# Kernel tuning notes

Hardware: AMD Instinct MI355X
Metric: run time of the kernel (lower is better)

## Reference

```python
import jax, jax.numpy as jnp
import numpy as np

H = 512          # HIDDEN_DIM
W = 480          # WINDOWWIDTH
NL = 8           # NUMLABELS (output_dim)
STEPS = W // 15  # 32 decoder steps
ATT = W // 16    # 30 attention positions
B = 4            # window batch
L = 12           # per-frame sequence length
D_IN = 32        # input_dim
N = B * W        # 1920 frame sequences


def _lstm(x, Wih, Whh, bih, bhh):
    # x: [T, Bn, Din] -> per-step hidden/cell states [T, Bn, Hd] (torch LSTM gate order i,f,g,o)
    xp = x @ Wih.T + (bih + bhh)
    h0 = jnp.zeros((x.shape[1], Whh.shape[1]), x.dtype)
    def step(carry, xt):
        h, c = carry
        g = xt + h @ Whh.T
        i, f, gg, o = jnp.split(g, 4, axis=-1)
        c = jax.nn.sigmoid(f) * c + jax.nn.sigmoid(i) * jnp.tanh(gg)
        h = jax.nn.sigmoid(o) * jnp.tanh(c)
        return (h, c), (h, c)
    _, (hs, cs) = jax.lax.scan(step, (h0, h0), xp)
    return hs, cs


def _bilstm(x, Wf, Uf, bf, cf, Wb, Ub, bb, cb):
    # x: [Bt, T, D] batch_first; returns ([Bt, T, 2H], h_fwd_final, h_bwd_final)
    xt = jnp.swapaxes(x, 0, 1)
    hf, _ = _lstm(xt, Wf, Uf, bf, cf)
    hb, _ = _lstm(xt[::-1], Wb, Ub, bb, cb)
    out = jnp.concatenate([hf, hb[::-1]], axis=-1)
    return jnp.swapaxes(out, 0, 1), hf[-1], hb[-1]


def _forward(xs, xlengths, enc_Wih, enc_Whh, enc_bih, enc_bhh,
             penc_Wih_f, penc_Whh_f, penc_bih_f, penc_bhh_f,
             penc_Wih_b, penc_Whh_b, penc_bih_b, penc_bhh_b,
             attn_W, attn_b, comb_W, comb_b,
             gru_Wih, gru_Whh, gru_bih, gru_bhh, out_W, out_b):
    # frame-level encoder: packed sequences -> (h, c) at each sequence's true length
    hs, cs = _lstm(xs, enc_Wih, enc_Whh, enc_bih, enc_bhh)   # [L, N, H] each
    idx = xlengths - 1
    ar = jnp.arange(N)
    ctx = jnp.concatenate([hs[idx, ar], cs[idx, ar]], axis=-1)  # [N, 2H]
    ctx = ctx.reshape(B, W // 2, 4 * H)
    # pyramidal BiLSTM stack (dropout is identity at eval)
    out = ctx
    hf = hb = None
    for i in range(4):
        out, hf, hb = _bilstm(ctx, penc_Wih_f[i], penc_Whh_f[i], penc_bih_f[i], penc_bhh_f[i],
                              penc_Wih_b[i], penc_Whh_b[i], penc_bih_b[i], penc_bhh_b[i])
        if i < 3:
            ctx = out.reshape(B, W // (2 ** (i + 2)), 4 * H)
    enc_out = out                                   # [B, ATT, 2H]
    hidden0 = jnp.concatenate([hf, hb], axis=-1)    # [B, 2H]

    def dstep(carry, _):
        inp, h = carry                              # [B, NL], [B, 2H]
        aw = jax.nn.softmax(jnp.concatenate([inp, h], axis=-1) @ attn_W.T + attn_b, axis=-1)
        ctxv = jnp.einsum('bt,btd->bd', aw, enc_out)
        x = jax.nn.relu(jnp.concatenate([inp, ctxv], axis=-1) @ comb_W.T + comb_b)
        # torch GRU cell (gate order r, z, n)
        gi = x @ gru_Wih.T + gru_bih
        gh = h @ gru_Whh.T + gru_bhh
        ir, iz, inn = jnp.split(gi, 3, axis=-1)
        hr, hz, hn = jnp.split(gh, 3, axis=-1)
        r = jax.nn.sigmoid(ir + hr)
        z = jax.nn.sigmoid(iz + hz)
        n = jnp.tanh(inn + r * hn)
        hnew = (1.0 - z) * n + z * h
        logp = jax.nn.log_softmax(hnew @ out_W.T + out_b, axis=-1)
        return (logp, hnew), logp                   # free-running: next input = log-probs

    inp0 = jnp.zeros((B, NL), xs.dtype)
    _, outs = jax.lax.scan(dstep, (inp0, hidden0), None, length=STEPS)  # [STEPS, B, NL]
    return jnp.swapaxes(outs, 0, 1).reshape(B * STEPS, NL)


def setup_inputs() -> dict:
    key = jax.random.key(0)
    ks = jax.random.split(key, 24)
    s = 0.03
    def nrm(k, shape):
        return jax.random.normal(k, shape, dtype=jnp.float32) * s
    return {
        'xs': jax.random.normal(ks[0], (L, N, D_IN), dtype=jnp.float32),
        'xlengths': jax.random.randint(ks[1], (N,), 1, L + 1, dtype=jnp.int32),
        'enc_Wih': nrm(ks[2], (4 * H, D_IN)),
        'enc_Whh': nrm(ks[3], (4 * H, H)),
        'enc_bih': nrm(ks[4], (4 * H,)),
        'enc_bhh': nrm(ks[5], (4 * H,)),
        'penc_Wih_f': nrm(ks[6], (4, 4 * H, 4 * H)),
        'penc_Whh_f': nrm(ks[7], (4, 4 * H, H)),
        'penc_bih_f': nrm(ks[8], (4, 4 * H)),
        'penc_bhh_f': nrm(ks[9], (4, 4 * H)),
        'penc_Wih_b': nrm(ks[10], (4, 4 * H, 4 * H)),
        'penc_Whh_b': nrm(ks[11], (4, 4 * H, H)),
        'penc_bih_b': nrm(ks[12], (4, 4 * H)),
        'penc_bhh_b': nrm(ks[13], (4, 4 * H)),
        'attn_W': nrm(ks[14], (ATT, 2 * H + NL)),
        'attn_b': nrm(ks[15], (ATT,)),
        'comb_W': nrm(ks[16], (H, 2 * H + NL)),
        'comb_b': nrm(ks[17], (H,)),
        'gru_Wih': nrm(ks[18], (3 * 2 * H, H)),
        'gru_Whh': nrm(ks[19], (3 * 2 * H, 2 * H)),
        'gru_bih': nrm(ks[20], (3 * 2 * H,)),
        'gru_bhh': nrm(ks[21], (3 * 2 * H,)),
        'out_W': nrm(ks[22], (NL, 2 * H)),
        'out_b': nrm(ks[23], (NL,)),
    }


def reference(xs, xlengths, enc_Wih, enc_Whh, enc_bih, enc_bhh,
              penc_Wih_f, penc_Whh_f, penc_bih_f, penc_bhh_f,
              penc_Wih_b, penc_Whh_b, penc_bih_b, penc_bhh_b,
              attn_W, attn_b, comb_W, comb_b,
              gru_Wih, gru_Whh, gru_bih, gru_bhh, out_W, out_b):
    return _forward(xs, xlengths, enc_Wih, enc_Whh, enc_bih, enc_bhh,
                    penc_Wih_f, penc_Whh_f, penc_bih_f, penc_bhh_f,
                    penc_Wih_b, penc_Whh_b, penc_bih_b, penc_bhh_b,
                    attn_W, attn_b, comb_W, comb_b,
                    gru_Wih, gru_Whh, gru_bih, gru_bhh, out_W, out_b)
```

## Files before the change

kernel.cpp:

```cpp
#include <hip/hip_runtime.h>
#include <stdint.h>

typedef __attribute__((ext_vector_type(8))) __bf16 bf16x8;
typedef __attribute__((ext_vector_type(4))) float f32x4;
typedef __attribute__((ext_vector_type(4))) unsigned u32x4;

#define DEVI static __device__ __forceinline__
#define SENT 0xFFFFFFFFu

DEVI bf16x8 bzero8(){ bf16x8 r;
#pragma unroll
  for (int i=0;i<8;++i) r[i]=(__bf16)0.0f; return r; }

DEVI bf16x8 ld8(const __bf16* p){ return *(const bf16x8*)p; }
DEVI void st8(__bf16* p, bf16x8 v){ *(bf16x8*)p = v; }

DEVI f32x4 MFMA(bf16x8 a, bf16x8 b, f32x4 c){
  return __builtin_amdgcn_mfma_f32_16x16x32_bf16(a, b, c, 0, 0, 0);
}

DEVI float sigf(float x){ return 1.0f/(1.0f+__expf(-x)); }

DEVI void ast(unsigned* p, unsigned v){ __hip_atomic_store(p, v, __ATOMIC_RELAXED, __HIP_MEMORY_SCOPE_AGENT); }

DEVI unsigned packbf(float a, float b){
  union { __bf16 h[2]; unsigned u; } x; x.h[0]=(__bf16)a; x.h[1]=(__bf16)b; return x.u;
}
DEVI float bflo(unsigned u){ return __builtin_bit_cast(float, u<<16); }
DEVI float bfhi(unsigned u){ return __builtin_bit_cast(float, u & 0xffff0000u); }

DEVI unsigned bad4(u32x4 v){ return (v[0]==SENT)|(v[1]==SENT)|(v[2]==SENT)|(v[3]==SENT); }

DEVI u32x4 ald4(const void* p){
  u32x4 v;
  asm volatile("global_load_dwordx4 %0, %1, off sc0 sc1\n\ts_waitcnt vmcnt(0)"
               : "=&v"(v) : "v"(p) : "memory");
  return v;
}
DEVI u32x4 poll4(const void* p){
  u32x4 v = ald4(p);
  while (bad4(v)){ __builtin_amdgcn_s_sleep(1); v = ald4(p); }
  return v;
}
DEVI void ald4x2(const void* p, u32x4& a, u32x4& b){
  asm volatile("global_load_dwordx4 %0, %2, off sc0 sc1\n\t"
               "global_load_dwordx4 %1, %2, off offset:16 sc0 sc1\n\t"
               "s_waitcnt vmcnt(0)"
               : "=&v"(a), "=&v"(b) : "v"(p) : "memory");
}
DEVI void poll4x2(const void* p, u32x4& a, u32x4& b){
  ald4x2(p, a, b);
  while (bad4(a) | bad4(b)){ __builtin_amdgcn_s_sleep(1); ald4x2(p, a, b); }
}

DEVI void packGroup(const float* W, int Nsrc, int Kreal, int NT, __bf16* dst, long g){
  int kt = (int)(g / (NT*64));
  int rem = (int)(g % (NT*64));
  int nt = rem >> 6, ln = rem & 63;
  int row = nt*16 + (ln & 15);
  int col = kt*32 + ((ln >> 4) << 3);
  bf16x8 v = bzero8();
  if (row < Nsrc){
#pragma unroll
    for (int j=0;j<8;++j){ int c = col + j; if (c < Kreal) v[j] = (__bf16)W[(long)row*Kreal + c]; }
  }
  st8(dst + g*8, v);
}

DEVI void packGroupCat(const float* Wih, const float* Whh, __bf16* dst, long g){
  int kt = (int)(g / (128*64));
  int rem = (int)(g % (128*64));
  int nt = rem >> 6, ln = rem & 63;
  int prow = nt*16 + (ln & 15);
  int src = (prow & 3)*512 + (prow >> 2);
  int col = kt*32 + ((ln >> 4) << 3);
  bf16x8 v;
  if (col < 32){
#pragma unroll
    for (int j=0;j<8;++j) v[j] = (__bf16)Wih[(long)src*32 + col + j];
  } else {
#pragma unroll
    for (int j=0;j<8;++j) v[j] = (__bf16)Whh[(long)src*512 + (col-32) + j];
  }
  st8(dst + g*8, v);
}

__global__ void initK(unsigned* hb){
  int g = blockIdx.x*256 + threadIdx.x;
  if (g < 6144) hb[2048 + g] = SENT;
}

__global__ void packSmallK(const float* __restrict__ xs, const float* __restrict__ eWih,
    const float* __restrict__ eWhh, const float* __restrict__ ebih, const float* __restrict__ ebhh,
    const float* __restrict__ attnW,
    __bf16* __restrict__ xsb, __bf16* __restrict__ wcatp, float* __restrict__ biasc,
    __bf16* __restrict__ attnp)
{
  long g = (long)blockIdx.x*blockDim.x + threadIdx.x;
  const long nWcat = 17L*128*64;
  const long nXs   = 92160;
  const long nBias = 2048;
  const long nAttn = 33L*2*64;
  if (g < nWcat){ packGroupCat(eWih, eWhh, wcatp, g); return; }
  g -= nWcat;
  if (g < nXs){
    const float* s = xs + g*8; bf16x8 v;
#pragma unroll
    for (int j=0;j<8;++j) v[j] = (__bf16)s[j];
    st8(xsb + g*8, v); return;
  }
  g -= nXs;
  if (g < nBias){ int src = ((int)g & 3)*512 + ((int)g >> 2); biasc[g] = ebih[src] + ebhh[src]; return; }
  g -= nBias;
  if (g < nAttn){ packGroup(attnW, 30, 1032, 2, attnp, g); return; }
}

__global__ void packPencK(const float* __restrict__ Wf, const float* __restrict__ Wb,
    const float* __restrict__ WhF, const float* __restrict__ WhB,
    const float* __restrict__ bihf, const float* __restrict__ bhhf,
    const float* __restrict__ bihb, const float* __restrict__ bhhb,
    __bf16* __restrict__ pf, __bf16* __restrict__ pb, float* __restrict__ bsum,
    __bf16* __restrict__ pwhh, unsigned* __restrict__ hpy)
{
  long g = (long)blockIdx.x*blockDim.x + threadIdx.x;
  const long nW = 64L*128*64;
  if (g < nW){ packGroup(Wf, 2048, 2048, 128, pf, g); return; }
  g -= nW;
  if (g < nW){ packGroup(Wb, 2048, 2048, 128, pb, g); return; }
  g -= nW;
  if (g < 2048){ bsum[g] = bihf[g] + bhhf[g]; return; }
  g -= 2048;
  if (g < 2048){ bsum[2048+g] = bihb[g] + bhhb[g]; return; }
  g -= 2048;
  if (g < 8192){
    hpy[g] = ((g >> 10) & 3) ? SENT : 0u;
    return;
  }
  g -= 8192;
  if (g < 262144){
    int lane = (int)(g & 63);
    int f    = (int)((g >> 6) & 31);
    int w    = (int)((g >> 11) & 3);
    int slot = (int)((g >> 13) & 15);
    int dir  = (int)((g >> 17) & 1);
    int kt = f >> 1, nt = f & 1;
    int row16 = lane & 15, kch = lane >> 4;
    int srow = w*512 + slot*32 + nt*16 + row16;
    int scol = kt*32 + kch*8;
    const float* W = dir ? WhB : WhF;
    bf16x8 v;
#pragma unroll
    for (int j=0;j<8;++j) v[j] = (__bf16)W[(long)srow*512 + scol + j];
    st8(pwhh + g*8, v);
  }
}

__global__ __launch_bounds__(256, 1) void encStepK(
    const __bf16* __restrict__ xsb,
    __bf16* __restrict__ henc,
    float* __restrict__ cenc,
    const __bf16* __restrict__ wcatp,
    const float* __restrict__ biasc,
    const int* __restrict__ xlen,
    __bf16* __restrict__ ctx,
    int t)
{
  __shared__ float glds[64][260];
  const int tid = threadIdx.x;
  const int w = tid >> 6, ln = tid & 63;
  const int m0 = blockIdx.x * 64;
  const int nb = blockIdx.y;
  f32x4 acc[16];
#pragma unroll
  for (int i=0;i<16;++i) acc[i] = (f32x4){0.f,0.f,0.f,0.f};

  const int arow = m0 + w*16 + (ln & 15);
  const int kc = (ln >> 4) << 3;
  const int ktEnd = (t == 0) ? 1 : 17;
  for (int kt = 0; kt < ktEnd; ++kt){
    bf16x8 a;
    if (kt == 0) a = ld8(xsb + ((long)t*1920 + arow)*32 + kc);
    else         a = ld8(henc + (long)arow*512 + (kt-1)*32 + kc);
    const __bf16* bp = wcatp + (((long)kt*128 + nb*16)*64 + ln)*8;
#pragma unroll
    for (int n2 = 0; n2 < 16; ++n2){
      bf16x8 b = ld8(bp + (long)n2*512);
      acc[n2] = MFMA(a, b, acc[n2]);
    }
  }
  const int r4 = (ln >> 4) << 2;
#pragma unroll
  for (int n2 = 0; n2 < 16; ++n2){
#pragma unroll
    for (int r = 0; r < 4; ++r)
      glds[w*16 + r4 + r][n2*16 + (ln & 15)] = acc[n2][r];
  }
  __syncthreads();
  for (int it = 0; it < 16; ++it){
    int idx = tid + it*256;
    int mrow = idx >> 6, hcl = idx & 63;
    int n = m0 + mrow;
    int hcg = nb*64 + hcl;
    float ig = glds[mrow][hcl*4+0] + biasc[nb*256 + hcl*4+0];
    float fg = glds[mrow][hcl*4+1] + biasc[nb*256 + hcl*4+1];
    float gg = glds[mrow][hcl*4+2] + biasc[nb*256 + hcl*4+2];
    float og = glds[mrow][hcl*4+3] + biasc[nb*256 + hcl*4+3];
    float c_old = (t == 0) ? 0.0f : cenc[(long)n*512 + hcg];
    float cn = sigf(fg)*c_old + sigf(ig)*tanhf(gg);
    float h  = sigf(og)*tanhf(cn);
    cenc[(long)n*512 + hcg] = cn;
    henc[(long)n*512 + hcg] = (__bf16)h;
    if (xlen[n] - 1 == t){
      ctx[(long)n*1024 + hcg]       = (__bf16)h;
      ctx[(long)n*1024 + 512 + hcg] = (__bf16)cn;
    }
  }
}

__global__ __launch_bounds__(1024) void pencInK(
   const __bf16* __restrict__ inb,
   const __bf16* __restrict__ wpf, const __bf16* __restrict__ wpb,
   const float* __restrict__ bsum,
   float* __restrict__ xpf, float* __restrict__ xpb,
   int M)
{
  const int tid = threadIdx.x, ln = tid & 63, wv = tid >> 6;
  const int rg = wv >> 2, cg = wv & 3;
  const int dir = blockIdx.z;
  const int m0 = blockIdx.x*64 + rg*16;
  const int nb = blockIdx.y;
  const __bf16* wp = dir ? wpb : wpf;
  float* xp = dir ? xpb : xpf;
  const float* bs = bsum + dir*2048;
  f32x4 acc[4];
#pragma unroll
  for (int i=0;i<4;++i) acc[i] = (f32x4){0.f,0.f,0.f,0.f};
  const int arow = m0 + (ln & 15);
  const int kc = (ln >> 4) << 3;
  const bool aok = arow < M;
  for (int kt = 0; kt < 64; ++kt){
    bf16x8 a = aok ? ld8(inb + (long)arow*2048 + kt*32 + kc) : bzero8();
    const __bf16* bp = wp + (((long)kt*128 + nb*16 + cg*4)*64 + ln)*8;
#pragma unroll
    for (int q = 0; q < 4; ++q){
      bf16x8 b = ld8(bp + (long)q*512);
      acc[q] = MFMA(a, b, acc[q]);
    }
  }
  const int r4 = (ln >> 4) << 2;
#pragma unroll
  for (int q = 0; q < 4; ++q){
    int col = (nb*16 + cg*4 + q)*16 + (ln & 15);
#pragma unroll
    for (int r = 0; r < 4; ++r){
      int rowo = m0 + r4 + r;
      if (rowo < M) xp[(long)rowo*2048 + col] = acc[q][r] + bs[col];
    }
  }
}

__global__ __launch_bounds__(256, 1) void pyrRecK(
  const __bf16* __restrict__ pwhh,
  const float* __restrict__ xpf, const float* __restrict__ xpb,
  __bf16* __restrict__ hbuf,
  __bf16* __restrict__ outb,
  float* __restrict__ outf,
  float* __restrict__ h0f, __bf16* __restrict__ h0b,
  int T, int isLast)
{
  __shared__ __align__(16) __bf16 hsL[2][4*512];
  __shared__ float glds[4][4][32];
  const int tid = threadIdx.x, ln = tid & 63, w = tid >> 6;
  const int bk = blockIdx.x;
  const int dir = bk >> 4, slot = bk & 15;
  const int hc0 = slot * 32;
  const float* xp = dir ? xpb : xpf;
  unsigned* hbu = (unsigned*)hbuf;

  bf16x8 BF[32];
  {
    const __bf16* wb = pwhh + ((((size_t)(dir*16 + slot)*4 + w)*32)*64 + ln)*8;
#pragma unroll
    for (int f = 0; f < 32; ++f) BF[f] = ld8(wb + (size_t)f*512);
  }

  const int arow = ln & 15;
  const int kc = (ln >> 4) << 3;
  float cv = 0.0f;
  float x0=0.f,x1=0.f,x2=0.f,x3=0.f;
  if (tid < 128){
    int pos0 = dir ? (T-1) : 0;
    const float* xr = xp + ((size_t)((tid>>5)*T + pos0))*2048 + hc0 + (tid & 31);
    x0 = xr[0]; x1 = xr[512]; x2 = xr[1024]; x3 = xr[1536];
  }

  for (int t = 0; t < T; ++t){
    int cur = t & 3, nxt = (t+1) & 3, clr = (t+2) & 3;
    int pos = dir ? (T-1-t) : t;
    {
      u32x4 v = poll4((const char*)hbuf + (size_t)(dir*4 + cur)*4096 + tid*16);
      ((u32x4*)hsL[t & 1])[tid] = v;
    }
    __syncthreads();
    if (tid < 64){
      int b = tid >> 4, i = tid & 15;
      ast(hbu + ((size_t)(dir*4 + clr)*4 + b)*256 + (hc0 >> 1) + i, SENT);
    }
    const __bf16* hs = hsL[t & 1];
    f32x4 a0 = {0.f,0.f,0.f,0.f}, a1 = a0, a2 = a0, a3 = a0;
#pragma unroll
    for (int kt = 0; kt < 16; kt += 2){
      bf16x8 aA = (arow < 4) ? ld8(hs + arow*512 + kt*32 + kc) : bzero8();
      bf16x8 aB = (arow < 4) ? ld8(hs + arow*512 + (kt+1)*32 + kc) : bzero8();
      a0 = MFMA(aA, BF[kt*2+0], a0);
      a1 = MFMA(aA, BF[kt*2+1], a1);
      a2 = MFMA(aB, BF[kt*2+2], a2);
      a3 = MFMA(aB, BF[kt*2+3], a3);
    }
    a0 += a2; a1 += a3;
    float xn0=0.f,xn1=0.f,xn2=0.f,xn3=0.f;
    if (t+1 < T && tid < 128){
      int pos2 = dir ? (T-2-t) : (t+1);
      const float* xr = xp + ((size_t)((tid>>5)*T + pos2))*2048 + hc0 + (tid & 31);
      xn0 = xr[0]; xn1 = xr[512]; xn2 = xr[1024]; xn3 = xr[1536];
    }
    if (ln < 16){
#pragma unroll
      for (int r=0;r<4;++r){ glds[w][r][ln] = a0[r]; glds[w][r][16+ln] = a1[r]; }
    }
    __syncthreads();
    if (tid < 128){
      int b = tid >> 5, hcl = tid & 31, hcg = hc0 + hcl;
      float ig = glds[0][b][hcl] + x0;
      float fg = glds[1][b][hcl] + x1;
      float gg = glds[2][b][hcl] + x2;
      float og = glds[3][b][hcl] + x3;
      cv = sigf(fg)*cv + sigf(ig)*tanhf(gg);
      float h = sigf(og)*tanhf(cv);
      float hn = __shfl_down(h, 1);
      if (!(hcl & 1))
        ast(hbu + ((size_t)(dir*4 + nxt)*4 + b)*256 + (hcg >> 1), packbf(h, hn));
      if (!isLast){
        outb[((long)(b*T + pos))*1024 + dir*512 + hcg] = (__bf16)h;
      } else {
        outf[((long)(b*T + pos))*1024 + dir*512 + hcg] = h;
        if (t == T-1){
          h0f[b*1024 + dir*512 + hcg] = h;
          h0b[b*1024 + dir*512 + hcg] = (__bf16)h;
        }
      }
    }
    x0=xn0; x1=xn1; x2=xn2; x3=xn3;
  }
}

__global__ __launch_bounds__(256) void precMK(const float* __restrict__ combW,
    const float* __restrict__ encOut, __bf16* __restrict__ Mb)
{
  __shared__ float eo[1024];
  int bt = blockIdx.x;
  int b = bt / 30, t = bt % 30;
  int tid = threadIdx.x;
  for (int i = tid; i < 1024; i += 256) eo[i] = encOut[((long)b*30 + t)*1024 + i];
  __syncthreads();
#pragma unroll 1
  for (int cc = 0; cc < 2; ++cc){
    int c = tid*2 + cc;
    const f32x4* wr4 = (const f32x4*)(combW + (long)c*1032 + 8);
    float s = 0.f;
    for (int d = 0; d < 256; ++d){
      f32x4 wv = wr4[d];
      s += wv[0]*eo[d*4] + wv[1]*eo[d*4+1] + wv[2]*eo[d*4+2] + wv[3]*eo[d*4+3];
    }
    Mb[((long)b*30 + t)*512 + c] = (__bf16)s;
  }
}

DEVI bf16x8 dfrag(const __bf16* base, const __bf16* inp, int row, int kt, int kc, int stride){
  if (row >= 4) return bzero8();
  int k = kt*32 + kc;
  if (k == 0) return ld8(inp + row*8);
  int off = k - 8;
  return (off < 1024) ? ld8(base + row*stride + off) : bzero8();
}

__global__ __launch_bounds__(256, 1) void decoderK(
  const float* __restrict__ gWih,
  const float* __restrict__ gWhh,
  const float* __restrict__ gbih, const float* __restrict__ gbhh,
  const float* __restrict__ combW,
  const float* __restrict__ combBias,
  const float* __restrict__ attnBias,
  const float* __restrict__ outW, const float* __restrict__ outBias,
  const __bf16* __restrict__ attnP,
  const __bf16* __restrict__ Mb,
  const float* __restrict__ h0f,
  __bf16* __restrict__ HB,
  float* __restrict__ dout)
{
  __shared__ __align__(16) __bf16 giL[96*512];
  __shared__ __align__(16) __bf16 outWL[8*1024];
  __shared__ __align__(16) __bf16 hL[4*1024];
  __shared__ __align__(16) __bf16 xL[4][520];
  __shared__ __align__(16) __bf16 WcIL[512][8];
  __shared__ __align__(16) __bf16 inpL[32];
  __shared__ float awL[4][32];
  __shared__ float redL[4][8];
  __shared__ float ghL[3][4][32];
  __shared__ float giO[3][4][32];
  __shared__ float biL[3][32], bhL[3][32];
  __shared__ float abL[30];
  __shared__ float cbAllL[512];

  const int tid = threadIdx.x, ln = tid & 63, w = tid >> 6;
  const int slot = blockIdx.x;
  const int hc0 = slot * 32;
  unsigned* HBu = (unsigned*)HB;

  for (int it = 0; it < 24; ++it){
    int g = it*256 + tid;
    int rho = g >> 6, c8 = g & 63;
    int gate = rho >> 5, r = rho & 31;
    const float* s = gWih + ((long)(gate*1024 + hc0 + r))*512 + c8*8;
    bf16x8 v;
#pragma unroll
    for (int j=0;j<8;++j) v[j] = (__bf16)s[j];
    st8((__bf16*)((char*)giL + ((rho*1024 + c8*16) ^ ((rho & 7) << 4))), v);
  }
  for (int it = 0; it < 32; ++it){
    int g = it*256 + tid;
    outWL[g] = (__bf16)outW[g];
  }
  for (int idx = tid; idx < 4096; idx += 256){
    int c = idx >> 3, j = idx & 7;
    WcIL[c][j] = (__bf16)combW[(long)c*1032 + j];
  }
  for (int idx = tid; idx < 512; idx += 256) cbAllL[idx] = combBias[idx];
  if (tid < 96){
    int g2 = tid >> 5, l = tid & 31;
    biL[g2][l] = gbih[g2*1024 + hc0 + l];
    bhL[g2][l] = gbhh[g2*1024 + hc0 + l];
  }
  if (tid < 30) abL[tid] = attnBias[tid];

  const int row = ln & 15, kc = (ln >> 4) << 3;
  bf16x8 bigF[66];
  if (w == 0){
#pragma unroll
    for (int nt = 0; nt < 2; ++nt)
#pragma unroll
      for (int kt = 0; kt < 33; ++kt)
        bigF[nt*33 + kt] = ld8(attnP + (((size_t)kt*2 + nt)*64 + ln)*8);
  } else {
    int gate = w - 1;
#pragma unroll
    for (int nt = 0; nt < 2; ++nt)
#pragma unroll
      for (int kt = 0; kt < 32; ++kt){
        const float* s = gWhh + ((long)(gate*1024 + hc0 + nt*16 + row))*1024 + kt*32 + kc;
        bf16x8 v;
#pragma unroll
        for (int j=0;j<8;++j) v[j] = (__bf16)s[j];
        bigF[nt*33 + kt] = v;
      }
  }

  float hold = 0.f;
  if (tid < 128) hold = h0f[(tid>>5)*1024 + hc0 + (tid & 31)];
  __syncthreads();

  for (int s = 0; s <= 32; ++s){
    int cur = s & 3, nxt = (s+1) & 3, clr = (s+2) & 3;
    {
      u32x4 q0, q1;
      poll4x2((const char*)HB + (size_t)cur*8192 + tid*32, q0, q1);
      ((u32x4*)hL)[tid*2]   = q0;
      ((u32x4*)hL)[tid*2+1] = q1;
    }
    __syncthreads();
    if (tid < 64){
      int b = tid >> 4, i = tid & 15;
      ast(HBu + ((size_t)clr*4 + b)*512 + (hc0 >> 1) + i, SENT);
    }
    if (s == 0){
      if (tid < 32) inpL[tid] = (__bf16)0.0f;
      __syncthreads();
    } else {
      int o = tid >> 3, sl = tid & 7;
      int b = o >> 3, l = o & 7;
      const unsigned* hlp = (const unsigned*)hL + b*512 + sl*64;
      const unsigned* wlp = (const unsigned*)outWL + l*512 + sl*64;
      float p = 0.f;
      for (int kk = 0; kk < 64; ++kk){
        unsigned u = hlp[kk], t2 = wlp[kk];
        p += bflo(u)*bflo(t2) + bfhi(u)*bfhi(t2);
      }
      p += __shfl_down(p, 4);
      p += __shfl_down(p, 2);
      p += __shfl_down(p, 1);
      if (sl == 0) redL[b][l] = p + outBias[l];
      __syncthreads();
      if (tid < 4){
        float m = redL[tid][0];
        for (int l2=1;l2<8;++l2) m = fmaxf(m, redL[tid][l2]);
        float sum = 0.f;
        for (int l2=0;l2<8;++l2) sum += __expf(redL[tid][l2]-m);
        float lse = m + __logf(sum);
        for (int l2=0;l2<8;++l2){
          float lp = redL[tid][l2] - lse;
          inpL[tid*8 + l2] = (__bf16)lp;
          if (slot == 0) dout[((long)tid*32 + (s-1))*8 + l2] = lp;
        }
      }
      __syncthreads();
    }
    if (s == 32) break;

    if (w == 0){
      f32x4 a0 = {0.f,0.f,0.f,0.f}, a1 = {0.f,0.f,0.f,0.f};
#pragma unroll
      for (int kt = 0; kt < 33; ++kt){
        bf16x8 a = dfrag(hL, inpL, row, kt, kc, 1024);
        a0 = MFMA(a, bigF[kt], a0);
        a1 = MFMA(a, bigF[33+kt], a1);
      }
      if (ln < 16){
#pragma unroll
        for (int r=0;r<4;++r) awL[r][ln] = a0[r] + abL[ln];
        if (16 + ln < 30){
#pragma unroll
          for (int r=0;r<4;++r) awL[r][16+ln] = a1[r] + abL[16+ln];
        }
      }
    } else {
      f32x4 a0 = {0.f,0.f,0.f,0.f}, a1 = {0.f,0.f,0.f,0.f};
#pragma unroll
      for (int kt = 0; kt < 32; ++kt){
        int k = kt*32 + kc;
        bf16x8 a = (row < 4) ? ld8(hL + row*1024 + k) : bzero8();
        a0 = MFMA(a, bigF[kt], a0);
        a1 = MFMA(a, bigF[33+kt], a1);
      }
      if (ln < 16){
        int gate = w - 1;
#pragma unroll
        for (int r=0;r<4;++r){
          ghL[gate][r][ln] = a0[r];
          ghL[gate][r][16+ln] = a1[r];
        }
      }
    }
    __syncthreads();
    if (tid < 4){
      float m = awL[tid][0];
      for (int t2=1;t2<30;++t2) m = fmaxf(m, awL[tid][t2]);
      float sum = 0.f;
      for (int t2=0;t2<30;++t2){ float e = __expf(awL[tid][t2]-m); awL[tid][t2] = e; sum += e; }
      float inv = 1.0f/sum;
      for (int t2=0;t2<30;++t2) awL[tid][t2] *= inv;
    }
    __syncthreads();
    {
      int c0 = tid*2;
#pragma unroll 1
      for (int b = 0; b < 4; ++b){
        float z0 = cbAllL[c0], z1 = cbAllL[c0+1];
#pragma unroll
        for (int j = 0; j < 8; ++j){
          float ij = (float)inpL[b*8 + j];
          z0 += (float)WcIL[c0][j]*ij;
          z1 += (float)WcIL[c0+1][j]*ij;
        }
        const unsigned* mp = (const unsigned*)Mb + (((long)b*30)*512 + c0)/2;
#pragma unroll
        for (int t2 = 0; t2 < 30; ++t2){
          unsigned u = mp[t2*256];
          float a = awL[b][t2];
          z0 += a*bflo(u);
          z1 += a*bfhi(u);
        }
        xL[b][c0]   = (__bf16)fmaxf(z0, 0.f);
        xL[b][c0+1] = (__bf16)fmaxf(z1, 0.f);
      }
    }
    __syncthreads();
    if (w >= 1){
      int gate = w - 1;
      f32x4 a0 = {0.f,0.f,0.f,0.f}, a1 = {0.f,0.f,0.f,0.f};
#pragma unroll
      for (int kt = 0; kt < 16; ++kt){
        int k = kt*32 + kc;
        bf16x8 a = (row < 4) ? ld8(&xL[row][k]) : bzero8();
        int r0 = gate*32 + row, r1 = r0 + 16;
        bf16x8 b0 = ld8((__bf16*)((char*)giL + ((r0*1024 + k*2) ^ ((r0 & 7) << 4))));
        bf16x8 b1 = ld8((__bf16*)((char*)giL + ((r1*1024 + k*2) ^ ((r1 & 7) << 4))));
        a0 = MFMA(a, b0, a0);
        a1 = MFMA(a, b1, a1);
      }
      if (ln < 16){
#pragma unroll
        for (int r=0;r<4;++r){
          giO[gate][r][ln] = a0[r] + biL[gate][ln];
          giO[gate][r][16+ln] = a1[r] + biL[gate][16+ln];
        }
      }
    }
    __syncthreads();
    if (tid < 128){
      int b = tid >> 5, l = tid & 31, hcg = hc0 + l;
      float rr = sigf(giO[0][b][l] + ghL[0][b][l] + bhL[0][l]);
      float zz = sigf(giO[1][b][l] + ghL[1][b][l] + bhL[1][l]);
      float nn = tanhf(giO[2][b][l] + rr*(ghL[2][b][l] + bhL[2][l]));
      float hnew = (1.0f - zz)*nn + zz*hold;
      hold = hnew;
      float h2 = __shfl_down(hnew, 1);
      if (!(l & 1))
        ast(HBu + ((size_t)nxt*4 + b)*512 + (hcg >> 1), packbf(hnew, h2));
    }
  }
}

static const size_t O_XSB   = 12288;
static const size_t O_WCATP = 1486848;
static const size_t O_BIASC = 3715072;
static const size_t O_HENC  = 3723264;
static const size_t O_PWHH  = 3723264;
static const size_t O_CENC  = 5689344;
static const size_t O_CTX   = 9621504;
static const size_t O_WIHPF = 13553664;
static const size_t O_WIHPB = 21942272;
static const size_t O_BSUM  = 30330880;
static const size_t O_XPF   = 30347264;
static const size_t O_XPB   = 38211584;
static const size_t O_HPYR  = 46075904;
static const size_t O_OUTA  = 46108672;
static const size_t O_OUTB  = 48074752;
static const size_t O_ENCO  = 49057792;
static const size_t O_H0F   = 49549312;
static const size_t O_HB    = 49565696;
static const size_t O_ATTNP = 49647616;
static const size_t O_M     = 49782784;

extern "C" void kernel_launch(void* const* d_in, const int* in_sizes, int n_in,
                              void* d_out, int out_size, void* d_ws, size_t ws_size,
                              hipStream_t stream)
{
  const float* xs    = (const float*)d_in[0];
  const int*   xlen  = (const int*)d_in[1];
  const float* eWih  = (const float*)d_in[2];
  const float* eWhh  = (const float*)d_in[3];
  const float* ebih  = (const float*)d_in[4];
  const float* ebhh  = (const float*)d_in[5];
  const float* pWihF = (const float*)d_in[6];
  const float* pWhhF = (const float*)d_in[7];
  const float* pbihF = (const float*)d_in[8];
  const float* pbhhF = (const float*)d_in[9];
  const float* pWihB = (const float*)d_in[10];
  const float* pWhhB = (const float*)d_in[11];
  const float* pbihB = (const float*)d_in[12];
  const float* pbhhB = (const float*)d_in[13];
  const float* attnW = (const float*)d_in[14];
  const float* attnb = (const float*)d_in[15];
  const float* combW = (const float*)d_in[16];
  const float* combb = (const float*)d_in[17];
  const float* gWih  = (const float*)d_in[18];
  const float* gWhh  = (const float*)d_in[19];
  const float* gbih  = (const float*)d_in[20];
  const float* gbhh  = (const float*)d_in[21];
  const float* outW  = (const float*)d_in[22];
  const float* outb  = (const float*)d_in[23];

  char* ws = (char*)d_ws;
  __bf16* XSB     = (__bf16*)(ws + O_XSB);
  __bf16* WCATP   = (__bf16*)(ws + O_WCATP);
  float*  BIASC   = (float*)(ws + O_BIASC);
  __bf16* HENC    = (__bf16*)(ws + O_HENC);
  __bf16* PWHH    = (__bf16*)(ws + O_PWHH);
  float*  CENC    = (float*)(ws + O_CENC);
  __bf16* CTX     = (__bf16*)(ws + O_CTX);
  __bf16* WIHPF   = (__bf16*)(ws + O_WIHPF);
  __bf16* WIHPB   = (__bf16*)(ws + O_WIHPB);
  float*  BSUM    = (float*)(ws + O_BSUM);
  float*  XPF     = (float*)(ws + O_XPF);
  float*  XPB     = (float*)(ws + O_XPB);
  __bf16* HPYR    = (__bf16*)(ws + O_HPYR);
  __bf16* OUTA    = (__bf16*)(ws + O_OUTA);
  __bf16* OUTB    = (__bf16*)(ws + O_OUTB);
  float*  ENCO    = (float*)(ws + O_ENCO);
  float*  H0F     = (float*)(ws + O_H0F);
  __bf16* HB      = (__bf16*)(ws + O_HB);
  __bf16* ATTNP   = (__bf16*)(ws + O_ATTNP);
  __bf16* MB      = (__bf16*)(ws + O_M);

  initK<<<24, 256, 0, stream>>>((unsigned*)HB);
  packSmallK<<<929, 256, 0, stream>>>(xs, eWih, eWhh, ebih, ebhh, attnW,
      XSB, WCATP, BIASC, ATTNP);

  for (int t = 0; t < 12; ++t)
    encStepK<<<dim3(30, 8), 256, 0, stream>>>(XSB, HENC, CENC, WCATP, BIASC, xlen, CTX, t);

  const int Ts[4] = {240, 120, 60, 30};
  const __bf16* ins[4] = {CTX, OUTA, OUTB, OUTA};
  __bf16* outs[4] = {OUTA, OUTB, OUTA, OUTB};
  for (int L = 0; L < 4; ++L){
    int T = Ts[L];
    packPencK<<<5168, 256, 0, stream>>>(pWihF + (long)L*2048*2048, pWihB + (long)L*2048*2048,
        pWhhF + (long)L*2048*512, pWhhB + (long)L*2048*512,
        pbihF + L*2048, pbhhF + L*2048, pbihB + L*2048, pbhhB + L*2048,
        WIHPF, WIHPB, BSUM, PWHH, (unsigned*)HPYR);
    int MBk = (4*T + 63)/64;
    pencInK<<<dim3(MBk, 8, 2), 1024, 0, stream>>>(ins[L], WIHPF, WIHPB, BSUM, XPF, XPB, 4*T);
    pyrRecK<<<32, 256, 0, stream>>>(PWHH, XPF, XPB, HPYR, outs[L], ENCO, H0F, HB,
        T, (L==3) ? 1 : 0);
  }

  precMK<<<120, 256, 0, stream>>>(combW, ENCO, MB);

  decoderK<<<32, 256, 0, stream>>>(gWih, gWhh, gbih, gbhh, combW, combb, attnb,
      outW, outb, ATTNP, MB, H0F, HB, (float*)d_out);
}
```

Baseline: 2.211 ms.

## Split GRU decoder across 64 blocks with prepacked bf16 weights streamed from global

The decoder now runs on 64 blocks, each owning 16 hidden units instead of 32, which halves the per-step MFMA work in each block. A new packDecK kernel converts the GRU Whh and Wih weights into MFMA-fragment bf16 layout ahead of time, reusing workspace regions of the pyramid input weights. The decoder no longer keeps Whh fragments in registers or Wih in LDS; it streams them from global/L2 every step, and the attention weights are likewise reloaded per step. This trades lower per-block latency and register pressure for extra global reads each step and more blocks taking part in the cross-block hidden-state exchange.

```diff
diff --git a/kernel.cpp b/kernel.cpp
--- a/kernel.cpp
+++ b/kernel.cpp
@@ -152,6 +152,37 @@
 #pragma unroll
     for (int j=0;j<8;++j) v[j] = (__bf16)W[(long)srow*512 + scol + j];
     st8(pwhh + g*8, v);
+  }
+}
+
+__global__ void packDecK(const float* __restrict__ gWhh, const float* __restrict__ gWih,
+    __bf16* __restrict__ pgh, __bf16* __restrict__ pgi)
+{
+  long g = (long)blockIdx.x*256 + threadIdx.x;
+  const long nGH = 192L*32*64;
+  const long nGI = 192L*16*64;
+  if (g < nGH){
+    int lane = (int)(g & 63); long idx = g >> 6;
+    int kt = (int)(idx & 31); int sg = (int)(idx >> 5);
+    int gate = sg % 3, slot = sg / 3;
+    int r = gate*1024 + slot*16 + (lane & 15);
+    int c = kt*32 + ((lane >> 4) << 3);
+    bf16x8 v;
+#pragma unroll
+    for (int j=0;j<8;++j) v[j] = (__bf16)gWhh[(long)r*1024 + c + j];
+    st8(pgh + g*8, v); return;
+  }
+  g -= nGH;
+  if (g < nGI){
+    int lane = (int)(g & 63); long idx = g >> 6;
+    int kt = (int)(idx & 15); int sg = (int)(idx >> 4);
+    int gate = sg % 3, slot = sg / 3;
+    int r = gate*1024 + slot*16 + (lane & 15);
+    int c = kt*32 + ((lane >> 4) << 3);
+    bf16x8 v;
+#pragma unroll
+    for (int j=0;j<8;++j) v[j] = (__bf16)gWih[(long)r*512 + c + j];
+    st8(pgi + g*8, v); return;
   }
 }
 
@@ -385,20 +416,19 @@
 }
 
 __global__ __launch_bounds__(256, 1) void decoderK(
-  const float* __restrict__ gWih,
-  const float* __restrict__ gWhh,
   const float* __restrict__ gbih, const float* __restrict__ gbhh,
   const float* __restrict__ combW,
   const float* __restrict__ combBias,
   const float* __restrict__ attnBias,
   const float* __restrict__ outW, const float* __restrict__ outBias,
   const __bf16* __restrict__ attnP,
+  const __bf16* __restrict__ pgh,
+  const __bf16* __restrict__ pgi,
   const __bf16* __restrict__ Mb,
   const float* __restrict__ h0f,
   __bf16* __restrict__ HB,
   float* __restrict__ dout)
 {
-  __shared__ __align__(16) __bf16 giL[96*512];
   __shared__ __align__(16) __bf16 outWL[8*1024];
   __shared__ __align__(16) __bf16 hL[4*1024];
   __shared__ __align__(16) __bf16 xL[4][520];
@@ -406,27 +436,17 @@
   __shared__ __align__(16) __bf16 inpL[32];
   __shared__ float awL[4][32];
   __shared__ float redL[4][8];
-  __shared__ float ghL[3][4][32];
-  __shared__ float giO[3][4][32];
-  __shared__ float biL[3][32], bhL[3][32];
+  __shared__ float ghL[3][4][16];
+  __shared__ float giO[3][4][16];
+  __shared__ float biL[3][16], bhL[3][16];
   __shared__ float abL[30];
   __shared__ float cbAllL[512];
 
   const int tid = threadIdx.x, ln = tid & 63, w = tid >> 6;
   const int slot = blockIdx.x;
-  const int hc0 = slot * 32;
+  const int hc0 = slot * 16;
   unsigned* HBu = (unsigned*)HB;
 
-  for (int it = 0; it < 24; ++it){
-    int g = it*256 + tid;
-    int rho = g >> 6, c8 = g & 63;
-    int gate = rho >> 5, r = rho & 31;
-    const float* s = gWih + ((long)(gate*1024 + hc0 + r))*512 + c8*8;
-    bf16x8 v;
-#pragma unroll
-    for (int j=0;j<8;++j) v[j] = (__bf16)s[j];
-    st8((__bf16*)((char*)giL + ((rho*1024 + c8*16) ^ ((rho & 7) << 4))), v);
-  }
   for (int it = 0; it < 32; ++it){
     int g = it*256 + tid;
     outWL[g] = (__bf16)outW[g];
@@ -436,37 +456,16 @@
     WcIL[c][j] = (__bf16)combW[(long)c*1032 + j];
   }
   for (int idx = tid; idx < 512; idx += 256) cbAllL[idx] = combBias[idx];
-  if (tid < 96){
-    int g2 = tid >> 5, l = tid & 31;
+  if (tid < 48){
+    int g2 = tid >> 4, l = tid & 15;
     biL[g2][l] = gbih[g2*1024 + hc0 + l];
     bhL[g2][l] = gbhh[g2*1024 + hc0 + l];
   }
   if (tid < 30) abL[tid] = attnBias[tid];
 
   const int row = ln & 15, kc = (ln >> 4) << 3;
-  bf16x8 bigF[66];
-  if (w == 0){
-#pragma unroll
-    for (int nt = 0; nt < 2; ++nt)
-#pragma unroll
-      for (int kt = 0; kt < 33; ++kt)
-        bigF[nt*33 + kt] = ld8(attnP + (((size_t)kt*2 + nt)*64 + ln)*8);
-  } else {
-    int gate = w - 1;
-#pragma unroll
-    for (int nt = 0; nt < 2; ++nt)
-#pragma unroll
-      for (int kt = 0; kt < 32; ++kt){
-        const float* s = gWhh + ((long)(gate*1024 + hc0 + nt*16 + row))*1024 + kt*32 + kc;
-        bf16x8 v;
-#pragma unroll
-        for (int j=0;j<8;++j) v[j] = (__bf16)s[j];
-        bigF[nt*33 + kt] = v;
-      }
-  }
-
   float hold = 0.f;
-  if (tid < 128) hold = h0f[(tid>>5)*1024 + hc0 + (tid & 31)];
+  if (tid < 64) hold = h0f[(tid>>4)*1024 + hc0 + (tid & 15)];
   __syncthreads();
 
   for (int s = 0; s <= 32; ++s){
@@ -478,8 +477,8 @@
       ((u32x4*)hL)[tid*2+1] = q1;
     }
     __syncthreads();
-    if (tid < 64){
-      int b = tid >> 4, i = tid & 15;
+    if (tid < 32){
+      int b = tid >> 3, i = tid & 7;
       ast(HBu + ((size_t)clr*4 + b)*512 + (hc0 >> 1) + i, SENT);
     }
     if (s == 0){
@@ -521,8 +520,10 @@
 #pragma unroll
       for (int kt = 0; kt < 33; ++kt){
         bf16x8 a = dfrag(hL, inpL, row, kt, kc, 1024);
-        a0 = MFMA(a, bigF[kt], a0);
-        a1 = MFMA(a, bigF[33+kt], a1);
+        bf16x8 b0 = ld8(attnP + (((size_t)kt*2 + 0)*64 + ln)*8);
+        bf16x8 b1 = ld8(attnP + (((size_t)kt*2 + 1)*64 + ln)*8);
+        a0 = MFMA(a, b0, a0);
+        a1 = MFMA(a, b1, a1);
       }
       if (ln < 16){
 #pragma unroll
@@ -533,21 +534,21 @@
         }
       }
     } else {
-      f32x4 a0 = {0.f,0.f,0.f,0.f}, a1 = {0.f,0.f,0.f,0.f};
-#pragma unroll
-      for (int kt = 0; kt < 32; ++kt){
+      int gate = w - 1;
+      const __bf16* bp = pgh + (((size_t)(slot*3 + gate)*32)*64 + ln)*8;
+      f32x4 a0 = {0.f,0.f,0.f,0.f}, a1 = a0;
+#pragma unroll
+      for (int kt = 0; kt < 32; kt += 2){
         int k = kt*32 + kc;
-        bf16x8 a = (row < 4) ? ld8(hL + row*1024 + k) : bzero8();
-        a0 = MFMA(a, bigF[kt], a0);
-        a1 = MFMA(a, bigF[33+kt], a1);
-      }
+        bf16x8 aA = (row < 4) ? ld8(hL + row*1024 + k) : bzero8();
+        bf16x8 aB = (row < 4) ? ld8(hL + row*1024 + k + 32) : bzero8();
+        a0 = MFMA(aA, ld8(bp + (size_t)kt*512), a0);
+        a1 = MFMA(aB, ld8(bp + (size_t)(kt+1)*512), a1);
+      }
+      a0 += a1;
       if (ln < 16){
-        int gate = w - 1;
-#pragma unroll
-        for (int r=0;r<4;++r){
-          ghL[gate][r][ln] = a0[r];
-          ghL[gate][r][16+ln] = a1[r];
-        }
+#pragma unroll
+        for (int r=0;r<4;++r) ghL[gate][r][ln] = a0[r];
       }
     }
     __syncthreads();
@@ -586,28 +587,25 @@
     __syncthreads();
     if (w >= 1){
       int gate = w - 1;
-      f32x4 a0 = {0.f,0.f,0.f,0.f}, a1 = {0.f,0.f,0.f,0.f};
-#pragma unroll
-      for (int kt = 0; kt < 16; ++kt){
+      const __bf16* bp = pgi + (((size_t)(slot*3 + gate)*16)*64 + ln)*8;
+      f32x4 a0 = {0.f,0.f,0.f,0.f}, a1 = a0;
+#pragma unroll
+      for (int kt = 0; kt < 16; kt += 2){
         int k = kt*32 + kc;
-        bf16x8 a = (row < 4) ? ld8(&xL[row][k]) : bzero8();
-        int r0 = gate*32 + row, r1 = r0 + 16;
-        bf16x8 b0 = ld8((__bf16*)((char*)giL + ((r0*1024 + k*2) ^ ((r0 & 7) << 4))));
-        bf16x8 b1 = ld8((__bf16*)((char*)giL + ((r1*1024 + k*2) ^ ((r1 & 7) << 4))));
-        a0 = MFMA(a, b0, a0);
-        a1 = MFMA(a, b1, a1);
-      }
+        bf16x8 aA = (row < 4) ? ld8(&xL[row][k]) : bzero8();
+        bf16x8 aB = (row < 4) ? ld8(&xL[row][k + 32]) : bzero8();
+        a0 = MFMA(aA, ld8(bp + (size_t)kt*512), a0);
+        a1 = MFMA(aB, ld8(bp + (size_t)(kt+1)*512), a1);
+      }
+      a0 += a1;
       if (ln < 16){
 #pragma unroll
-        for (int r=0;r<4;++r){
-          giO[gate][r][ln] = a0[r] + biL[gate][ln];
-          giO[gate][r][16+ln] = a1[r] + biL[gate][16+ln];
-        }
+        for (int r=0;r<4;++r) giO[gate][r][ln] = a0[r] + biL[gate][ln];
       }
     }
     __syncthreads();
-    if (tid < 128){
-      int b = tid >> 5, l = tid & 31, hcg = hc0 + l;
+    if (tid < 64){
+      int b = tid >> 4, l = tid & 15, hcg = hc0 + l;
       float rr = sigf(giO[0][b][l] + ghL[0][b][l] + bhL[0][l]);
       float zz = sigf(giO[1][b][l] + ghL[1][b][l] + bhL[1][l]);
       float nn = tanhf(giO[2][b][l] + rr*(ghL[2][b][l] + bhL[2][l]));
@@ -628,7 +626,9 @@
 static const size_t O_CENC  = 5689344;
 static const size_t O_CTX   = 9621504;
 static const size_t O_WIHPF = 13553664;
+static const size_t O_PGH   = 13553664;
 static const size_t O_WIHPB = 21942272;
+static const size_t O_PGI   = 21942272;
 static const size_t O_BSUM  = 30330880;
 static const size_t O_XPF   = 30347264;
 static const size_t O_XPB   = 38211584;
@@ -680,6 +680,8 @@
   __bf16* CTX     = (__bf16*)(ws + O_CTX);
   __bf16* WIHPF   = (__bf16*)(ws + O_WIHPF);
   __bf16* WIHPB   = (__bf16*)(ws + O_WIHPB);
+  __bf16* PGH     = (__bf16*)(ws + O_PGH);
+  __bf16* PGI     = (__bf16*)(ws + O_PGI);
   float*  BSUM    = (float*)(ws + O_BSUM);
   float*  XPF     = (float*)(ws + O_XPF);
   float*  XPB     = (float*)(ws + O_XPB);
@@ -710,12 +712,14 @@
         WIHPF, WIHPB, BSUM, PWHH, (unsigned*)HPYR);
     int MBk = (4*T + 63)/64;
     pencInK<<<dim3(MBk, 8, 2), 1024, 0, stream>>>(ins[L], WIHPF, WIHPB, BSUM, XPF, XPB, 4*T);
+    if (L == 3)
+      packDecK<<<2304, 256, 0, stream>>>(gWhh, gWih, PGH, PGI);
     pyrRecK<<<32, 256, 0, stream>>>(PWHH, XPF, XPB, HPYR, outs[L], ENCO, H0F, HB,
         T, (L==3) ? 1 : 0);
   }
 
   precMK<<<120, 256, 0, stream>>>(combW, ENCO, MB);
 
-  decoderK<<<32, 256, 0, stream>>>(gWih, gWhh, gbih, gbhh, combW, combb, attnb,
-      outW, outb, ATTNP, MB, H0F, HB, (float*)d_out);
-}
+  decoderK<<<64, 256, 0, stream>>>(gbih, gbhh, combW, combb, attnb, outW, outb,
+      ATTNP, PGH, PGI, MB, H0F, HB, (float*)d_out);
+}
```

Measured after the change: 2.397 ms. +8.4%, slower.
